# Kernel optimization log

Measured on AMD Instinct MI355X. Metric: run time of the kernel, lower is better.

Reference implementation:

```python
import jax, jax.numpy as jnp
import numpy as np

N, E, G, H, L = 50000, 400000, 2000, 128, 5
NPG = N // G  # 25 nodes per graph
EPS = 1e-5    # PNA std epsilon
D_LOG = 1.0   # avg_d['log'] as in 3DInfomax PNAGNN


def setup_inputs():
    key = jax.random.key(0)
    ks = jax.random.split(key, 32)
    node_feat = jax.random.randint(ks[0], (N, 9), 0, 16)
    edge_feat = jax.random.randint(ks[1], (E, 3), 0, 5)
    src = jax.random.randint(ks[2], (E,), 0, N)
    off = jax.random.randint(ks[3], (E,), 1, NPG)
    # dst stays in the same graph as src and differs from src
    dst = (src // NPG) * NPG + (src % NPG + off) % NPG
    graph_id = jnp.arange(N) // NPG
    inp = dict(node_feat=node_feat, edge_feat=edge_feat, src=src, dst=dst,
               graph_id=graph_id)
    shapes = [("aemb_f", (144, H)), ("bemb_f", (15, H)),
              ("w_pre_f", (L, 3 * H, H)), ("b_pre_f", (L, H)),
              ("w_post_f", (L, 13 * H, H)), ("b_post_f", (L, H)),
              ("w_out3", (3 * H, 256)), ("b_out3", (256,)),
              ("aemb", (144, H)), ("bemb", (15, H)),
              ("w_pre", (L, 3 * H, H)), ("b_pre", (L, H)),
              ("w_post", (L, 13 * H, H)), ("b_post", (L, H)),
              ("w1", (3 * H + 256, H)), ("b1", (H,)),
              ("w2", (H, 128)), ("b2", (128,))]
    for i, (n, s) in enumerate(shapes):
        inp[n] = jax.random.normal(ks[4 + i], s, dtype=jnp.float32) * 0.05
    return inp


def _embed(table, x, vocab):
    # sum of per-feature embeddings (OGB Atom/Bond encoder)
    idx = x + jnp.arange(x.shape[1]) * vocab
    return table[idx].sum(axis=1)


def _pna_gnn(aemb, bemb, w_pre, b_pre, w_post, b_post,
             node_feat, edge_feat, src, dst):
    h = _embed(aemb, node_feat, 16)   # [N, H]
    e = _embed(bemb, edge_feat, 5)    # [E, H]
    deg = jax.ops.segment_sum(jnp.ones((src.shape[0],), jnp.float32), dst, N)
    safe_deg = jnp.maximum(deg, 1.0)[:, None]
    log_deg = jnp.log(deg + 1.0)[:, None]
    amp = log_deg / D_LOG                                   # amplification scaler
    att = jnp.where(log_deg > 0, D_LOG / jnp.where(log_deg > 0, log_deg, 1.0), 0.0)
    has_in = (deg > 0)[:, None]
    for l in range(L):
        h_in = h
        # pretrans over edges: cat(src, dst, edge) -> linear (pretrans_layers=1, last_activation='none')
        z = jnp.concatenate([h[src], h[dst], e], axis=-1) @ w_pre[l] + b_pre[l]  # [E, H]
        s1 = jax.ops.segment_sum(z, dst, N)
        mean = s1 / safe_deg
        mean_sq = jax.ops.segment_sum(z * z, dst, N) / safe_deg
        std = jnp.sqrt(jax.nn.relu(mean_sq - mean * mean) + EPS)
        mx = jnp.where(has_in, jax.ops.segment_max(z, dst, N), 0.0)
        mn = jnp.where(has_in, jax.ops.segment_min(z, dst, N), 0.0)
        agg = jnp.concatenate([mean, mx, mn, std], axis=-1)          # [N, 4H]
        f = jnp.concatenate([agg, agg * amp, agg * att], axis=-1)    # [N, 12H]
        f = jnp.where(has_in, f, 0.0)  # DGL leaves zero-in-degree nodes at zero
        h = jnp.concatenate([h, f], axis=-1) @ w_post[l] + b_post[l]
        h = h + h_in  # residual
    return h


def _readout(h, graph_id):
    mean = jax.ops.segment_sum(h, graph_id, G) / NPG
    mx = jax.ops.segment_max(h, graph_id, G)
    mn = jax.ops.segment_min(h, graph_id, G)
    return jnp.concatenate([mn, mx, mean], axis=-1)  # order: min, max, mean


def reference(aemb_f, bemb_f, w_pre_f, b_pre_f, w_post_f, b_post_f,
              w_out3, b_out3, aemb, bemb, w_pre, b_pre, w_post, b_post,
              w1, b1, w2, b2, node_feat, edge_feat, src, dst, graph_id):
    # frozen 3D branch (torch.no_grad + detach -> stop_gradient)
    h3 = _pna_gnn(aemb_f, bemb_f, w_pre_f, b_pre_f, w_post_f, b_post_f,
                  node_feat, edge_feat, src, dst)
    r3 = _readout(h3, graph_id)
    latent3d = jax.lax.stop_gradient(r3 @ w_out3 + b_out3)  # [G, 256]
    # trainable 2D branch
    h2 = _pna_gnn(aemb, bemb, w_pre, b_pre, w_post, b_post,
                  node_feat, edge_feat, src, dst)
    r2 = _readout(h2, graph_id)                              # [G, 384]
    x = jnp.concatenate([r2, latent3d], axis=-1)             # [G, 640]
    h1 = jax.nn.relu(x @ w1 + b1)
    return h1 @ w2 + b2                                      # [G, 128]
```

## Files before the change

### kernel.cpp

```cpp
#include <hip/hip_runtime.h>
#include <hip/hip_bf16.h>
#include <math.h>

#define Nn 50000
#define Ee 400000
#define Gg 2000
#define NPGc 25
#define Hc 128
#define Lc 5
#define M2c 50048
#define R2c 100096

typedef __attribute__((ext_vector_type(8))) short short8;
typedef __attribute__((ext_vector_type(4))) float fx4;

__device__ inline short bf16r(float x){
  unsigned u = __float_as_uint(x);
  unsigned r = (u + 0x7fffu + ((u >> 16) & 1u)) >> 16;
  return (short)r;
}
__device__ inline float bf16f(short s){
  return __uint_as_float(((unsigned)(unsigned short)s) << 16);
}

__global__ void deg_kernel(const int* __restrict__ dst, int* __restrict__ deg, int E){
  int i = blockIdx.x * blockDim.x + threadIdx.x;
  if (i < E) atomicAdd(&deg[dst[i]], 1);
}

__global__ void scan1_kernel(const int* __restrict__ deg, int* __restrict__ part,
                             int* __restrict__ bsums, int n){
  __shared__ int tmp[1024];
  int b = blockIdx.x, t = threadIdx.x;
  int i = b * 1024 + t;
  int v = (i < n) ? deg[i] : 0;
  tmp[t] = v;
  __syncthreads();
  for (int off = 1; off < 1024; off <<= 1){
    int add = (t >= off) ? tmp[t - off] : 0;
    __syncthreads();
    tmp[t] += add;
    __syncthreads();
  }
  part[i] = tmp[t];
  if (t == 1023) bsums[b] = tmp[1023];
}
__global__ void scan2_kernel(int* __restrict__ bsums, int nb){
  if (threadIdx.x == 0){
    int s = 0;
    for (int i = 0; i < nb; i++){ s += bsums[i]; bsums[i] = s; }
  }
}
__global__ void scan3_kernel(const int* __restrict__ part, const int* __restrict__ bsums,
                             int* __restrict__ rowstart, int n){
  int i = blockIdx.x * blockDim.x + threadIdx.x;
  if (i == 0) rowstart[0] = 0;
  if (i < n){
    int b = i >> 10;
    int base = b ? bsums[b - 1] : 0;
    rowstart[i + 1] = part[i] + base;
  }
}

__global__ void copy_int_kernel(const int* __restrict__ a, int* __restrict__ b, int n){
  int i = blockIdx.x * blockDim.x + threadIdx.x;
  if (i < n) b[i] = a[i];
}

__global__ void scatter_kernel(const int* __restrict__ src, const int* __restrict__ dst,
                               const int* __restrict__ ef, int* cursor,
                               int* __restrict__ pk_srt, int E){
  int i = blockIdx.x * blockDim.x + threadIdx.x;
  if (i >= E) return;
  int p = atomicAdd(&cursor[dst[i]], 1);
  int code = ef[i * 3 + 0] * 25 + ef[i * 3 + 1] * 5 + ef[i * 3 + 2];
  pk_srt[p] = (code << 16) | (src[i] % NPGc);
}

__global__ void ampatt_kernel(const int* __restrict__ deg, float* __restrict__ amp,
                              float* __restrict__ att, int n){
  int i = blockIdx.x * blockDim.x + threadIdx.x;
  if (i >= n) return;
  if (i >= Nn){ amp[i] = 0.f; att[i] = 0.f; return; }
  float d = (float)deg[i];
  float ld = logf(d + 1.0f);
  amp[i] = ld;
  att[i] = (deg[i] > 0) ? (1.0f / ld) : 0.0f;
}

__global__ void embed2_kernel(const int* __restrict__ nf,
                              const float* __restrict__ aemb_f,
                              const float* __restrict__ aemb_t,
                              float* __restrict__ h, short* __restrict__ h16){
  int idx = blockIdx.x * blockDim.x + threadIdx.x;
  if (idx >= R2c * Hc) return;
  int n = idx >> 7, c = idx & 127;
  int br = n >= M2c;
  int local = n - br * M2c;
  if (local >= Nn){ h[idx] = 0.f; h16[idx] = 0; return; }
  const float* aemb = br ? aemb_t : aemb_f;
  float s = 0.f;
#pragma unroll
  for (int f = 0; f < 9; f++){
    int row = nf[local * 9 + f] + 16 * f;
    s += aemb[row * Hc + c];
  }
  h[idx] = s;
  h16[idx] = bf16r(s);
}

__global__ void bsum2_kernel(const float* __restrict__ bemb_f, const float* __restrict__ bemb_t,
                             float* __restrict__ bsum2){
  int idx = blockIdx.x * blockDim.x + threadIdx.x;
  if (idx >= 2 * 125 * Hc) return;
  int b = idx / (125 * Hc);
  int rem = idx % (125 * Hc);
  int code = rem >> 7, c = rem & 127;
  int e0 = code / 25, e1 = (code / 5) % 5, e2 = code % 5;
  const float* bemb = b ? bemb_t : bemb_f;
  bsum2[idx] = bemb[e0 * Hc + c] + bemb[(5 + e1) * Hc + c] + bemb[(10 + e2) * Hc + c];
}

__global__ void conv_pre_all_kernel(const float* __restrict__ wpre_f,
                                    const float* __restrict__ wpre_t,
                                    short* __restrict__ btpre_all){
  int idx = blockIdx.x * blockDim.x + threadIdx.x;
  if (idx >= 2 * Lc * 256 * 128) return;
  int bl = idx / (256 * 128);
  int rem = idx % (256 * 128);
  int col = rem >> 7, k = rem & 127;
  int b = bl / Lc, l = bl % Lc;
  const float* wl = (b ? wpre_t : wpre_f) + (size_t)l * 384 * 128;
  float v = (col < 128) ? wl[k * 128 + col] : wl[(128 + k) * 128 + (col - 128)];
  btpre_all[(size_t)bl * 256 * 128 + col * 128 + k] = bf16r(v);
}
__global__ void conv_post_all_kernel(const float* __restrict__ wpost_f,
                                     const float* __restrict__ wpost_t,
                                     short* __restrict__ btpost_all){
  int idx = blockIdx.x * blockDim.x + threadIdx.x;
  if (idx >= 2 * Lc * 1664 * 128) return;
  int bl = idx / (1664 * 128);
  int rem = idx % (1664 * 128);
  int k = rem >> 7, c = rem & 127;
  int b = bl / Lc, l = bl % Lc;
  const float* wl = (b ? wpost_t : wpost_f) + (size_t)l * 1664 * 128;
  btpost_all[(size_t)bl * 128 * 1664 + (size_t)c * 1664 + k] = bf16r(wl[(size_t)k * 128 + c]);
}

__global__ void ezt_all_kernel(const float* __restrict__ wpre_f, const float* __restrict__ wpre_t,
                               const float* __restrict__ bpre_f, const float* __restrict__ bpre_t,
                               const float* __restrict__ bsum2, short* __restrict__ ezt16_all){
  int code = blockIdx.x;
  int bl   = blockIdx.y;
  int t = threadIdx.x;
  int b = bl / Lc, l = bl % Lc;
  const float* wl = (b ? wpre_t : wpre_f) + (size_t)l * 384 * 128 + 256 * 128;
  const float* bp = (b ? bpre_t : bpre_f) + (size_t)l * 128;
  __shared__ float bs[128];
  bs[t] = bsum2[((size_t)b * 125 + code) * 128 + t];
  __syncthreads();
  float acc = bp[t];
#pragma unroll 8
  for (int k = 0; k < 128; k++) acc += bs[k] * wl[k * 128 + t];
  ezt16_all[((size_t)bl * 125 + code) * 128 + t] = bf16r(acc);
}

__global__ void readout2_kernel(const float* __restrict__ h,
                                float* __restrict__ r3, float* __restrict__ r2){
  int bi = blockIdx.x;
  int br = bi >= Gg;
  int g = bi - br * Gg;
  int c = threadIdx.x;
  float mn = 3.402823466e38f, mx = -3.402823466e38f, s = 0.f;
  const float* hp = h + ((size_t)br * M2c + (size_t)g * NPGc) * Hc + c;
#pragma unroll
  for (int i = 0; i < NPGc; i++){
    float v = hp[i * Hc];
    mn = fminf(mn, v); mx = fmaxf(mx, v); s += v;
  }
  float* r = br ? r2 : r3;
  r[(size_t)g * 384 + c]       = mn;
  r[(size_t)g * 384 + 128 + c] = mx;
  r[(size_t)g * 384 + 256 + c] = s * (1.0f / NPGc);
}

__global__ __launch_bounds__(256)
void head_kernel(const float* __restrict__ r2, const float* __restrict__ r3,
                 const float* __restrict__ w_out3, const float* __restrict__ b_out3,
                 const float* __restrict__ w1, const float* __restrict__ b1,
                 const float* __restrict__ w2, const float* __restrict__ b2,
                 float* __restrict__ out)
{
  __shared__ float r3_s[384];
  __shared__ float x_s[640];
  __shared__ float h1_s[128];
  __shared__ float partial[256];
  int g = blockIdx.x, t = threadIdx.x;

  for (int i = t; i < 384; i += 256){
    float v2 = r2[(size_t)g * 384 + i];
    r3_s[i] = r3[(size_t)g * 384 + i];
    x_s[i] = v2;
  }
  __syncthreads();

  {
    float acc = b_out3[t];
#pragma unroll 8
    for (int k = 0; k < 384; k++) acc += r3_s[k] * w_out3[k * 256 + t];
    x_s[384 + t] = acc;
  }
  __syncthreads();

  {
    int c = t & 127, half = t >> 7;
    float acc = half ? 0.f : b1[c];
    int kb = half * 320;
#pragma unroll 8
    for (int k = kb; k < kb + 320; k++) acc += x_s[k] * w1[k * 128 + c];
    partial[t] = acc;
  }
  __syncthreads();
  if (t < 128) h1_s[t] = fmaxf(partial[t] + partial[t + 128], 0.f);
  __syncthreads();

  {
    int c = t & 127, half = t >> 7;
    float acc = half ? 0.f : b2[c];
    int kb = half * 64;
#pragma unroll 8
    for (int k = kb; k < kb + 64; k++) acc += h1_s[k] * w2[k * 128 + c];
    partial[t] = acc;
  }
  __syncthreads();
  if (t < 128) out[(size_t)g * 128 + t] = partial[t] + partial[t + 128];
}

__global__ __launch_bounds__(256)
void mgemm0_kernel(const short* __restrict__ A16,
                   const short* __restrict__ Bt,
                   short* __restrict__ C16)
{
  const int K = 128, NC = 256;
  __shared__ short8 As[512];
  __shared__ short8 Bs[1024];

  int tid = threadIdx.x;
  int row0 = blockIdx.y * 64;
  int col0 = blockIdx.x * 128;
  int wv = tid >> 6, ln = tid & 63;
  int lo = ln & 15, q = ln >> 4;

  int a_rq = (tid >> 6) & 3, a_q = (tid >> 4) & 3, a_lo = tid & 15;
  int a_grow = row0 + a_rq * 16 + a_lo;
  int b_q = (tid >> 4) & 3, b_lo = tid & 15, b_ct0 = (tid >> 6) & 3;

  fx4 acc[8];
#pragma unroll
  for (int ct = 0; ct < 8; ct++) acc[ct] = (fx4){0.f, 0.f, 0.f, 0.f};

  short8 ra[2], rb[4];
  auto loadA = [&](int k0){
#pragma unroll
    for (int i = 0; i < 2; i++)
      ra[i] = *(const short8*)(A16 + (size_t)a_grow * 128 + k0 + i * 32 + a_q * 8);
  };
  auto loadB = [&](int k0){
#pragma unroll
    for (int i = 0; i < 4; i++){
      int ct = b_ct0 + (i & 1) * 4;
      int col = col0 + ct * 16 + b_lo;
      int gk = k0 + (i >> 1) * 32 + b_q * 8;
      rb[i] = *(const short8*)(Bt + (size_t)col * K + gk);
    }
  };

  loadA(0); loadB(0);
  for (int k0 = 0; k0 < K; k0 += 64){
    __syncthreads();
#pragma unroll
    for (int i = 0; i < 2; i++) As[i * 256 + tid] = ra[i];
#pragma unroll
    for (int i = 0; i < 4; i++) Bs[i * 256 + tid] = rb[i];
    __syncthreads();
    int kn = k0 + 64;
    if (kn < K){ loadA(kn); loadB(kn); }
    short8 a0 = As[wv * 64 + ln];
    short8 a1 = As[256 + wv * 64 + ln];
#pragma unroll
    for (int ct = 0; ct < 8; ct++){
      short8 b0 = Bs[ct * 64 + ln];
      short8 b1 = Bs[512 + ct * 64 + ln];
      acc[ct] = __builtin_amdgcn_mfma_f32_16x16x32_bf16(a0, b0, acc[ct], 0, 0, 0);
      acc[ct] = __builtin_amdgcn_mfma_f32_16x16x32_bf16(a1, b1, acc[ct], 0, 0, 0);
    }
  }

#pragma unroll
  for (int r = 0; r < 4; r++){
    int row = row0 + wv * 16 + q * 4 + r;
#pragma unroll
    for (int ct = 0; ct < 8; ct++){
      int col = col0 + ct * 16 + lo;
      C16[(size_t)row * NC + col] = bf16r(acc[ct][r]);
    }
  }
}

__global__ __launch_bounds__(256)
void agg_kernel(const int* __restrict__ hsdP,
                const int* __restrict__ ez16,
                const int* __restrict__ pk_srt, const int* __restrict__ rowstart,
                short* __restrict__ aggOut)
{
  __shared__ int hs_s[NPGc * 64];
  int tid = threadIdx.x;
  int base = blockIdx.x * NPGc;

  for (int t = tid; t < NPGc * 64; t += 256){
    int nd = t >> 6, off = t & 63;
    hs_s[t] = hsdP[(size_t)(base + nd) * 128 + off];
  }
  __syncthreads();

  int sub = tid & 15;
  int go = sub * 4;

#pragma unroll
  for (int rnd = 0; rnd < 2; rnd++){
    int nd = rnd * 16 + (tid >> 4);
    if (nd >= NPGc) continue;
    int node = base + nd;
    int e0 = rowstart[node], e1 = rowstart[node + 1];
    short* o = aggOut + (size_t)node * 512 + sub * 8;
    if (e1 <= e0){
      short8 z = {0, 0, 0, 0, 0, 0, 0, 0};
      *(short8*)(o)       = z;
      *(short8*)(o + 128) = z;
      *(short8*)(o + 256) = z;
      *(short8*)(o + 384) = z;
      continue;
    }

    float hdv[8];
    {
      int4 hd = *(const int4*)(hsdP + (size_t)node * 128 + 64 + go);
      const int* hp = (const int*)&hd;
#pragma unroll
      for (int i = 0; i < 4; i++){
        hdv[2 * i]     = __uint_as_float(((unsigned)hp[i]) << 16);
        hdv[2 * i + 1] = __uint_as_float(((unsigned)hp[i]) & 0xffff0000u);
      }
    }

    float sum[8], sq[8], mx[8], mn[8];
#pragma unroll
    for (int j = 0; j < 8; j++){
      sum[j] = 0.f; sq[j] = 0.f;
      mx[j] = -3.402823466e38f; mn[j] = 3.402823466e38f;
    }

    for (int k = e0; k < e1; k += 4){
      int pk[4];
#pragma unroll
      for (int t2 = 0; t2 < 4; t2++){
        int kk = (k + t2 < e1) ? (k + t2) : (e1 - 1);
        pk[t2] = pk_srt[kk];
      }
      int4 ev[4], hv[4];
#pragma unroll
      for (int t2 = 0; t2 < 4; t2++){
        ev[t2] = *(const int4*)(ez16 + (pk[t2] >> 16) * 64 + go);
        hv[t2] = *(const int4*)(hs_s + (pk[t2] & 0xffff) * 64 + go);
      }
#pragma unroll
      for (int t2 = 0; t2 < 4; t2++){
        if (k + t2 < e1){
          const int* pp = (const int*)&hv[t2];
          const int* ee = (const int*)&ev[t2];
#pragma unroll
          for (int i = 0; i < 4; i++){
            float z0 = __uint_as_float(((unsigned)pp[i]) << 16) + hdv[2 * i]
                     + __uint_as_float(((unsigned)ee[i]) << 16);
            float z1 = __uint_as_float(((unsigned)pp[i]) & 0xffff0000u) + hdv[2 * i + 1]
                     + __uint_as_float(((unsigned)ee[i]) & 0xffff0000u);
            sum[2 * i] += z0;     sq[2 * i] += z0 * z0;
            mx[2 * i] = fmaxf(mx[2 * i], z0); mn[2 * i] = fminf(mn[2 * i], z0);
            sum[2 * i + 1] += z1; sq[2 * i + 1] += z1 * z1;
            mx[2 * i + 1] = fmaxf(mx[2 * i + 1], z1); mn[2 * i + 1] = fminf(mn[2 * i + 1], z1);
          }
        }
      }
    }

    float d = (float)(e1 - e0);
    float rd = 1.0f / d;
    short8 sm, sx, sn, sd;
#pragma unroll
    for (int j = 0; j < 8; j++){
      float m = sum[j] * rd;
      float v = sq[j] * rd - m * m; v = v > 0.f ? v : 0.f;
      sm[j] = bf16r(m);
      sx[j] = bf16r(mx[j]);
      sn[j] = bf16r(mn[j]);
      sd[j] = bf16r(sqrtf(v + 1e-5f));
    }
    *(short8*)(o)       = sm;
    *(short8*)(o + 128) = sx;
    *(short8*)(o + 256) = sn;
    *(short8*)(o + 384) = sd;
  }
}

__global__ __launch_bounds__(256, 4)
void post_gemm_kernel(const short* __restrict__ A16,
                      const short* __restrict__ aggG,
                      const short* __restrict__ Bt0, const short* __restrict__ Bt1,
                      const float* __restrict__ bias0, const float* __restrict__ bias1,
                      const float* __restrict__ amp, const float* __restrict__ att,
                      const float* __restrict__ resid,
                      float* __restrict__ C, short* __restrict__ C16)
{
  __shared__ short8 As[1024];
  __shared__ short8 Bs[1024];

  int tid = threadIdx.x;
  int row0 = blockIdx.x * 128;
  int br = row0 >= M2c;
  const short* Bt = br ? Bt1 : Bt0;
  const float* bias = br ? bias1 : bias0;
  int wv = tid >> 6, ln = tid & 63;
  int lo = ln & 15, q = ln >> 4;

  int a_rq = (tid >> 6) & 3, a_q = (tid >> 4) & 3, a_lo = tid & 15;
  int b_q = (tid >> 4) & 3, b_lo = tid & 15, b_ct0 = (tid >> 6) & 3;

  int arow[2]; float ampv[2], attv[2];
#pragma unroll
  for (int j = 0; j < 2; j++){
    arow[j] = row0 + (a_rq + 4 * j) * 16 + a_lo;
    int lr = arow[j] - br * M2c;
    ampv[j] = amp[lr]; attv[j] = att[lr];
  }
  int colb[2];
#pragma unroll
  for (int j = 0; j < 2; j++) colb[j] = ((b_ct0 + 4 * j) * 16 + b_lo) * 1664;

  fx4 acc[2][8];
#pragma unroll
  for (int j = 0; j < 2; j++)
#pragma unroll
    for (int ct = 0; ct < 8; ct++) acc[j][ct] = (fx4){0.f, 0.f, 0.f, 0.f};

  short8 ra[2][2], rb[2][2];
  auto loadA = [&](int s){
    if (s < 2){
#pragma unroll
      for (int i = 0; i < 2; i++){
        int k = s * 64 + i * 32 + a_q * 8;
#pragma unroll
        for (int j = 0; j < 2; j++)
          ra[i][j] = *(const short8*)(A16 + (size_t)arow[j] * 128 + k);
      }
    } else {
      int kc = (s - 2) / 3;
#pragma unroll
      for (int i = 0; i < 2; i++){
        int koff = kc * 64 + i * 32 + a_q * 8;
#pragma unroll
        for (int j = 0; j < 2; j++)
          ra[i][j] = *(const short8*)(aggG + (size_t)arow[j] * 512 + koff);
      }
    }
  };
  auto loadB = [&](int s){
    int gkb;
    if (s < 2) gkb = s * 64;
    else {
      int t = s - 2, kc = t / 3, ph = t % 3;
      gkb = (ph == 0 ? 128 : (ph == 1 ? 640 : 1152)) + kc * 64;
    }
#pragma unroll
    for (int i = 0; i < 2; i++){
      int gk = gkb + i * 32 + b_q * 8;
#pragma unroll
      for (int j = 0; j < 2; j++)
        rb[i][j] = *(const short8*)(Bt + (size_t)colb[j] + gk);
    }
  };

  loadA(0); loadB(0);
  for (int s = 0; s < 26; s++){
    int ph = (s < 2) ? 0 : (s - 2) % 3;
    __syncthreads();
    if (ph == 0){
#pragma unroll
      for (int i = 0; i < 2; i++)
#pragma unroll
        for (int j = 0; j < 2; j++) As[i * 512 + j * 256 + tid] = ra[i][j];
    } else {
#pragma unroll
      for (int i = 0; i < 2; i++)
#pragma unroll
        for (int j = 0; j < 2; j++){
          float sc = (ph == 1) ? ampv[j] : attv[j];
          short8 v = ra[i][j];
#pragma unroll
          for (int e = 0; e < 8; e++)
            ((short*)&v)[e] = bf16r(bf16f(((short*)&v)[e]) * sc);
          As[i * 512 + j * 256 + tid] = v;
        }
    }
#pragma unroll
    for (int i = 0; i < 2; i++)
#pragma unroll
      for (int j = 0; j < 2; j++) Bs[i * 512 + j * 256 + tid] = rb[i][j];
    __syncthreads();
    if (s < 25){
      loadB(s + 1);
      if (s + 1 < 2 || (s - 1) % 3 == 0) loadA(s + 1);
    }
    short8 a00 = As[wv * 64 + ln];
    short8 a10 = As[512 + wv * 64 + ln];
    short8 a01 = As[256 + wv * 64 + ln];
    short8 a11 = As[768 + wv * 64 + ln];
#pragma unroll
    for (int ct = 0; ct < 8; ct++){
      short8 b0 = Bs[ct * 64 + ln];
      short8 b1 = Bs[512 + ct * 64 + ln];
      acc[0][ct] = __builtin_amdgcn_mfma_f32_16x16x32_bf16(a00, b0, acc[0][ct], 0, 0, 0);
      acc[0][ct] = __builtin_amdgcn_mfma_f32_16x16x32_bf16(a10, b1, acc[0][ct], 0, 0, 0);
      acc[1][ct] = __builtin_amdgcn_mfma_f32_16x16x32_bf16(a01, b0, acc[1][ct], 0, 0, 0);
      acc[1][ct] = __builtin_amdgcn_mfma_f32_16x16x32_bf16(a11, b1, acc[1][ct], 0, 0, 0);
    }
  }

#pragma unroll
  for (int j = 0; j < 2; j++){
#pragma unroll
    for (int ct = 0; ct < 8; ct++){
      int col = ct * 16 + lo;
      float bcol = bias[col];
#pragma unroll
      for (int r = 0; r < 4; r++){
        int row = row0 + (wv + 4 * j) * 16 + q * 4 + r;
        float v = acc[j][ct][r] + bcol + resid[(size_t)row * 128 + col];
        C[(size_t)row * 128 + col] = v;
        C16[(size_t)row * 128 + col] = bf16r(v);
      }
    }
  }
}

extern "C" void kernel_launch(void* const* d_in, const int* in_sizes, int n_in,
                              void* d_out, int out_size, void* d_ws, size_t ws_size,
                              hipStream_t stream)
{
  const int*   node_feat = (const int*)  d_in[0];
  const int*   edge_feat = (const int*)  d_in[1];
  const int*   src       = (const int*)  d_in[2];
  const int*   dst       = (const int*)  d_in[3];
  const float* aemb_f  = (const float*) d_in[5];
  const float* bemb_f  = (const float*) d_in[6];
  const float* w_pre_f = (const float*) d_in[7];
  const float* b_pre_f = (const float*) d_in[8];
  const float* w_post_f= (const float*) d_in[9];
  const float* b_post_f= (const float*) d_in[10];
  const float* w_out3  = (const float*) d_in[11];
  const float* b_out3  = (const float*) d_in[12];
  const float* aemb    = (const float*) d_in[13];
  const float* bemb    = (const float*) d_in[14];
  const float* w_pre   = (const float*) d_in[15];
  const float* b_pre   = (const float*) d_in[16];
  const float* w_post  = (const float*) d_in[17];
  const float* b_post  = (const float*) d_in[18];
  const float* w1      = (const float*) d_in[19];
  const float* b1      = (const float*) d_in[20];
  const float* w2      = (const float*) d_in[21];
  const float* b2      = (const float*) d_in[22];
  float* out = (float*)d_out;

  char* w = (char*)d_ws;
  auto carve = [&](size_t bytes) -> void* {
    void* p = (void*)w;
    w += (bytes + 255) & ~(size_t)255;
    return p;
  };
  float* h         = (float*)carve((size_t)R2c * Hc * 4);
  short* h16       = (short*)carve((size_t)R2c * Hc * 2);
  short* hsd16     = (short*)carve((size_t)M2c * 256 * 2);
  short* aggG      = (short*)carve((size_t)R2c * 512 * 2);
  short* btpre_all = (short*)carve((size_t)2 * Lc * 256 * 128 * 2);
  short* btpost_all= (short*)carve((size_t)2 * Lc * 128 * 1664 * 2);
  short* ezt16_all = (short*)carve((size_t)2 * Lc * 125 * Hc * 2);
  float* amp       = (float*)carve((size_t)M2c * 4);
  float* att       = (float*)carve((size_t)M2c * 4);
  int* rowstart = (int*)carve((size_t)(Nn + 1) * 4);
  int* pk_srt   = (int*)carve((size_t)Ee * 4);

  char* ali = (char*)aggG;
  float* r3     = (float*)(ali);
  float* r2     = (float*)(ali + (size_t)4 * 1024 * 1024);
  int*   deg    = (int*)  (ali + (size_t)8 * 1024 * 1024);
  int*   cursor = (int*)  (ali + (size_t)9 * 1024 * 1024);
  int*   part   = (int*)  (ali + (size_t)10 * 1024 * 1024);
  int*   bsums  = (int*)  (ali + (size_t)11 * 1024 * 1024);
  float* bsum2  = (float*)(ali + (size_t)12 * 1024 * 1024);

  hipMemsetAsync(deg, 0, (size_t)Nn * 4, stream);
  deg_kernel<<<(Ee + 255) / 256, 256, 0, stream>>>(dst, deg, Ee);
  scan1_kernel<<<49, 1024, 0, stream>>>(deg, part, bsums, Nn);
  scan2_kernel<<<1, 64, 0, stream>>>(bsums, 49);
  scan3_kernel<<<(Nn + 255) / 256, 256, 0, stream>>>(part, bsums, rowstart, Nn);
  copy_int_kernel<<<(Nn + 255) / 256, 256, 0, stream>>>(rowstart, cursor, Nn);
  scatter_kernel<<<(Ee + 255) / 256, 256, 0, stream>>>(src, dst, edge_feat, cursor,
                                                       pk_srt, Ee);
  ampatt_kernel<<<(M2c + 255) / 256, 256, 0, stream>>>(deg, amp, att, M2c);

  hipMemsetAsync(aggG + (size_t)Nn * 512, 0, (size_t)(M2c - Nn) * 512 * 2, stream);
  hipMemsetAsync(aggG + ((size_t)M2c + Nn) * 512, 0, (size_t)(M2c - Nn) * 512 * 2, stream);

  bsum2_kernel<<<(2 * 125 * Hc + 255) / 256, 256, 0, stream>>>(bemb_f, bemb, bsum2);
  conv_pre_all_kernel<<<(2 * Lc * 256 * 128 + 255) / 256, 256, 0, stream>>>(
      w_pre_f, w_pre, btpre_all);
  conv_post_all_kernel<<<(2 * Lc * 1664 * 128 + 255) / 256, 256, 0, stream>>>(
      w_post_f, w_post, btpost_all);
  ezt_all_kernel<<<dim3(125, 2 * Lc), 128, 0, stream>>>(
      w_pre_f, w_pre, b_pre_f, b_pre, bsum2, ezt16_all);

  embed2_kernel<<<(R2c * Hc + 255) / 256, 256, 0, stream>>>(
      node_feat, aemb_f, aemb, h, h16);

  for (int l = 0; l < Lc; l++){
    const short* pre0 = btpre_all + (size_t)(0 * Lc + l) * 256 * 128;
    const short* pre1 = btpre_all + (size_t)(1 * Lc + l) * 256 * 128;
    const short* post0 = btpost_all + (size_t)(0 * Lc + l) * 128 * 1664;
    const short* post1 = btpost_all + (size_t)(1 * Lc + l) * 128 * 1664;
    const int* ez0 = (const int*)(ezt16_all + (size_t)(0 * Lc + l) * 125 * Hc);
    const int* ez1 = (const int*)(ezt16_all + (size_t)(1 * Lc + l) * 125 * Hc);
    const float* bp0 = b_post_f + (size_t)l * 128;
    const float* bp1 = b_post   + (size_t)l * 128;

    mgemm0_kernel<<<dim3(2, M2c / 64), 256, 0, stream>>>(
        h16, pre0, hsd16);
    agg_kernel<<<Gg, 256, 0, stream>>>(
        (const int*)hsd16, ez0, pk_srt, rowstart, aggG);

    mgemm0_kernel<<<dim3(2, M2c / 64), 256, 0, stream>>>(
        h16 + (size_t)M2c * 128, pre1, hsd16);
    agg_kernel<<<Gg, 256, 0, stream>>>(
        (const int*)hsd16, ez1, pk_srt, rowstart, aggG + (size_t)M2c * 512);

    post_gemm_kernel<<<R2c / 128, 256, 0, stream>>>(
        h16, aggG, post0, post1, bp0, bp1, amp, att, h, h, h16);
  }

  readout2_kernel<<<2 * Gg, 128, 0, stream>>>(h, r3, r2);
  head_kernel<<<Gg, 256, 0, stream>>>(r2, r3, w_out3, b_out3, w1, b1, w2, b2, out);
}
```

Before: 1.416 ms.

## Fuse pre-transform GEMM into per-graph aggregation kernel using shared-memory tiles

Merges the separate pre-transform GEMM and edge aggregation kernels into one kernel per graph. Each block loads its 25 nodes' features into swizzled LDS, computes the 256-wide src/dst projections with MFMA directly into LDS, then aggregates edges from LDS. This removes the global round trip of the hsd intermediate and halves kernel launches per layer. In exchange, the GEMM pads 25 rows to 32, and each block re-reads the full weight matrix from global/L2. The larger LDS footprint may also reduce occupancy.

```diff
diff --git a/kernel.cpp b/kernel.cpp
--- a/kernel.cpp
+++ b/kernel.cpp
@@ -236,95 +236,77 @@
   if (t < 128) out[(size_t)g * 128 + t] = partial[t] + partial[t + 128];
 }
 
-__global__ __launch_bounds__(256)
-void mgemm0_kernel(const short* __restrict__ A16,
-                   const short* __restrict__ Bt,
-                   short* __restrict__ C16)
+__global__ __launch_bounds__(256, 4)
+void fgemm_agg_kernel(const short* __restrict__ h16b,
+                      const short* __restrict__ Bt,
+                      const int* __restrict__ ez16,
+                      const int* __restrict__ pk_srt, const int* __restrict__ rowstart,
+                      short* __restrict__ aggOut)
 {
-  const int K = 128, NC = 256;
-  __shared__ short8 As[512];
-  __shared__ short8 Bs[1024];
+  __shared__ short h_s[32 * 128];
+  __shared__ short hsd_s[32 * 256];
 
   int tid = threadIdx.x;
-  int row0 = blockIdx.y * 64;
-  int col0 = blockIdx.x * 128;
+  int g = blockIdx.x;
+  int base = g * NPGc;
+
+  {
+    const int* src = (const int*)(h16b + (size_t)base * 128);
+    int* dst = (int*)h_s;
+    for (int t = tid; t < NPGc * 64; t += 256){
+      int row = t >> 6, ci = t & 63;
+      dst[row * 64 + (ci ^ ((row & 7) << 2))] = src[t];
+    }
+  }
+  __syncthreads();
+
   int wv = tid >> 6, ln = tid & 63;
-  int lo = ln & 15, q = ln >> 4;
-
-  int a_rq = (tid >> 6) & 3, a_q = (tid >> 4) & 3, a_lo = tid & 15;
-  int a_grow = row0 + a_rq * 16 + a_lo;
-  int b_q = (tid >> 4) & 3, b_lo = tid & 15, b_ct0 = (tid >> 6) & 3;
-
-  fx4 acc[8];
-#pragma unroll
-  for (int ct = 0; ct < 8; ct++) acc[ct] = (fx4){0.f, 0.f, 0.f, 0.f};
-
-  short8 ra[2], rb[4];
-  auto loadA = [&](int k0){
-#pragma unroll
-    for (int i = 0; i < 2; i++)
-      ra[i] = *(const short8*)(A16 + (size_t)a_grow * 128 + k0 + i * 32 + a_q * 8);
-  };
-  auto loadB = [&](int k0){
-#pragma unroll
-    for (int i = 0; i < 4; i++){
-      int ct = b_ct0 + (i & 1) * 4;
-      int col = col0 + ct * 16 + b_lo;
-      int gk = k0 + (i >> 1) * 32 + b_q * 8;
-      rb[i] = *(const short8*)(Bt + (size_t)col * K + gk);
-    }
-  };
-
-  loadA(0); loadB(0);
-  for (int k0 = 0; k0 < K; k0 += 64){
-    __syncthreads();
-#pragma unroll
-    for (int i = 0; i < 2; i++) As[i * 256 + tid] = ra[i];
-#pragma unroll
-    for (int i = 0; i < 4; i++) Bs[i * 256 + tid] = rb[i];
-    __syncthreads();
-    int kn = k0 + 64;
-    if (kn < K){ loadA(kn); loadB(kn); }
-    short8 a0 = As[wv * 64 + ln];
-    short8 a1 = As[256 + wv * 64 + ln];
-#pragma unroll
-    for (int ct = 0; ct < 8; ct++){
-      short8 b0 = Bs[ct * 64 + ln];
-      short8 b1 = Bs[512 + ct * 64 + ln];
-      acc[ct] = __builtin_amdgcn_mfma_f32_16x16x32_bf16(a0, b0, acc[ct], 0, 0, 0);
-      acc[ct] = __builtin_amdgcn_mfma_f32_16x16x32_bf16(a1, b1, acc[ct], 0, 0, 0);
-    }
-  }
-
-#pragma unroll
-  for (int r = 0; r < 4; r++){
-    int row = row0 + wv * 16 + q * 4 + r;
-#pragma unroll
-    for (int ct = 0; ct < 8; ct++){
-      int col = col0 + ct * 16 + lo;
-      C16[(size_t)row * NC + col] = bf16r(acc[ct][r]);
-    }
-  }
-}
-
-__global__ __launch_bounds__(256)
-void agg_kernel(const int* __restrict__ hsdP,
-                const int* __restrict__ ez16,
-                const int* __restrict__ pk_srt, const int* __restrict__ rowstart,
-                short* __restrict__ aggOut)
-{
-  __shared__ int hs_s[NPGc * 64];
-  int tid = threadIdx.x;
-  int base = blockIdx.x * NPGc;
-
-  for (int t = tid; t < NPGc * 64; t += 256){
-    int nd = t >> 6, off = t & 63;
-    hs_s[t] = hsdP[(size_t)(base + nd) * 128 + off];
+  int l15 = ln & 15, lq = ln >> 4;
+  {
+    fx4 acc[2][4];
+#pragma unroll
+    for (int mt = 0; mt < 2; mt++)
+#pragma unroll
+      for (int ct = 0; ct < 4; ct++) acc[mt][ct] = (fx4){0.f, 0.f, 0.f, 0.f};
+
+    short8 af[2][4];
+#pragma unroll
+    for (int mt = 0; mt < 2; mt++){
+      int row = mt * 16 + l15;
+#pragma unroll
+      for (int ks = 0; ks < 4; ks++){
+        int sk = ks * 32 + lq * 8;
+        af[mt][ks] = *(const short8*)(h_s + row * 128 + (sk ^ ((row & 7) << 3)));
+      }
+    }
+#pragma unroll
+    for (int ks = 0; ks < 4; ks++){
+#pragma unroll
+      for (int ct = 0; ct < 4; ct++){
+        int col = wv * 64 + ct * 16 + l15;
+        short8 bf = *(const short8*)(Bt + (size_t)col * 128 + ks * 32 + lq * 8);
+        acc[0][ct] = __builtin_amdgcn_mfma_f32_16x16x32_bf16(af[0][ks], bf, acc[0][ct], 0, 0, 0);
+        acc[1][ct] = __builtin_amdgcn_mfma_f32_16x16x32_bf16(af[1][ks], bf, acc[1][ct], 0, 0, 0);
+      }
+    }
+#pragma unroll
+    for (int mt = 0; mt < 2; mt++){
+#pragma unroll
+      for (int ct = 0; ct < 4; ct++){
+        int cc = wv * 64 + ct * 16 + l15;
+#pragma unroll
+        for (int r = 0; r < 4; r++){
+          int row = mt * 16 + lq * 4 + r;
+          hsd_s[row * 256 + (cc ^ ((row & 7) << 3))] = bf16r(acc[mt][ct][r]);
+        }
+      }
+    }
   }
   __syncthreads();
 
   int sub = tid & 15;
   int go = sub * 4;
+  const int* hsd_i = (const int*)hsd_s;
 
 #pragma unroll
   for (int rnd = 0; rnd < 2; rnd++){
@@ -344,7 +326,7 @@
 
     float hdv[8];
     {
-      int4 hd = *(const int4*)(hsdP + (size_t)node * 128 + 64 + go);
+      int4 hd = *(const int4*)(hsd_i + nd * 128 + ((64 + go) ^ ((nd & 7) << 2)));
       const int* hp = (const int*)&hd;
 #pragma unroll
       for (int i = 0; i < 4; i++){
@@ -370,8 +352,9 @@
       int4 ev[4], hv[4];
 #pragma unroll
       for (int t2 = 0; t2 < 4; t2++){
+        int s = pk[t2] & 0xffff;
         ev[t2] = *(const int4*)(ez16 + (pk[t2] >> 16) * 64 + go);
-        hv[t2] = *(const int4*)(hs_s + (pk[t2] & 0xffff) * 64 + go);
+        hv[t2] = *(const int4*)(hsd_i + s * 128 + (go ^ ((s & 7) << 2)));
       }
 #pragma unroll
       for (int t2 = 0; t2 < 4; t2++){
@@ -588,7 +571,6 @@
   };
   float* h         = (float*)carve((size_t)R2c * Hc * 4);
   short* h16       = (short*)carve((size_t)R2c * Hc * 2);
-  short* hsd16     = (short*)carve((size_t)M2c * 256 * 2);
   short* aggG      = (short*)carve((size_t)R2c * 512 * 2);
   short* btpre_all = (short*)carve((size_t)2 * Lc * 256 * 128 * 2);
   short* btpost_all= (short*)carve((size_t)2 * Lc * 128 * 1664 * 2);
@@ -641,15 +623,11 @@
     const float* bp0 = b_post_f + (size_t)l * 128;
     const float* bp1 = b_post   + (size_t)l * 128;
 
-    mgemm0_kernel<<<dim3(2, M2c / 64), 256, 0, stream>>>(
-        h16, pre0, hsd16);
-    agg_kernel<<<Gg, 256, 0, stream>>>(
-        (const int*)hsd16, ez0, pk_srt, rowstart, aggG);
-
-    mgemm0_kernel<<<dim3(2, M2c / 64), 256, 0, stream>>>(
-        h16 + (size_t)M2c * 128, pre1, hsd16);
-    agg_kernel<<<Gg, 256, 0, stream>>>(
-        (const int*)hsd16, ez1, pk_srt, rowstart, aggG + (size_t)M2c * 512);
+    fgemm_agg_kernel<<<Gg, 256, 0, stream>>>(
+        h16, pre0, ez0, pk_srt, rowstart, aggG);
+    fgemm_agg_kernel<<<Gg, 256, 0, stream>>>(
+        h16 + (size_t)M2c * 128, pre1, ez1, pk_srt, rowstart,
+        aggG + (size_t)M2c * 512);
 
     post_gemm_kernel<<<R2c / 128, 256, 0, stream>>>(
         h16, aggG, post0, post1, bp0, bp1, amp, att, h, h, h16);
```

Measured after the change: 1.379 ms. 1.03x faster.
